# Optimization experiments

Hardware: AMD Instinct MI355X
Metric: run time of the kernel (lower is better)

Reference implementation:

```python
import jax, jax.numpy as jnp
import numpy as np

B, H = 4096, 1024
N1, N2, N3 = 28, 280, 2800  # nodes (== classes == paths) per level, branching [28,10,10]


def setup_inputs() -> dict:
    key = jax.random.key(0)
    ks = jax.random.split(key, 8)
    s = 1.0 / np.sqrt(H)  # torch nn.Linear default init bound
    x = jax.random.normal(ks[0], (B, H), jnp.float32)
    labels = jax.random.randint(ks[1], (B,), 0, N3, dtype=jnp.int32)
    W1 = jax.random.uniform(ks[2], (N1, H), jnp.float32, -s, s)
    b1 = jax.random.uniform(ks[3], (N1,), jnp.float32, -s, s)
    W2 = jax.random.uniform(ks[4], (N2, H), jnp.float32, -s, s)
    b2 = jax.random.uniform(ks[5], (N2,), jnp.float32, -s, s)
    W3 = jax.random.uniform(ks[6], (N3, H), jnp.float32, -s, s)
    b3 = jax.random.uniform(ks[7], (N3,), jnp.float32, -s, s)
    return {"x": x, "labels": labels, "W1": W1, "b1": b1,
            "W2": W2, "b2": b2, "W3": W3, "b3": b3}


def _ce(logits, lab):
    # mean cross-entropy, same as torch.nn.CrossEntropyLoss (mean reduction)
    lp = jax.nn.log_softmax(logits, axis=-1)
    return -jnp.take_along_axis(lp, lab[:, None], axis=1).mean()


def reference(x, labels, W1, b1, W2, b2, W3, b3):
    # per-level node probabilities: one grouped GEMM per level replaces the
    # Python loop of tiny Linear(hidden,1)+sigmoid calls
    z1 = jax.nn.sigmoid(x @ W1.T + b1)  # [B, N1]
    z2 = jax.nn.sigmoid(x @ W2.T + b2)  # [B, N2]
    z3 = jax.nn.sigmoid(x @ W3.T + b3)  # [B, N3]

    # path (prefix) matrices: leaf k has path [k//100, k//10, k].
    # NOTE: all nodes of a path index into the CURRENT level's weights,
    # exactly as self.nodes[lvl][node] does in the source.
    i2 = jnp.arange(N2)
    p2 = jnp.stack([i2 // 10, i2], axis=1)                    # [N2, 2]
    i3 = jnp.arange(N3)
    p3 = jnp.stack([i3 // 100, i3 // 10, i3], axis=1)          # [N3, 3]

    logits1 = z1                                               # prod over length-1 path
    logits2 = jnp.prod(z2[:, p2], axis=-1)                     # [B, N2]
    logits3 = jnp.prod(z3[:, p3], axis=-1)                     # [B, N3]

    # update_label_per_lvl: label -> ancestor node id at that level
    lab1 = labels // 100
    lab2 = labels // 10
    loss = _ce(logits1, lab1) + _ce(logits2, lab2) + _ce(logits3, labels)
    return logits3, loss
```

## Files before the change

kernel.cpp:

```cpp
#include <hip/hip_runtime.h>
#include <cstdint>


typedef unsigned short u16;
typedef unsigned char u8;
typedef long i64;
typedef float f32x4 __attribute__((ext_vector_type(4)));

#define AS_G __attribute__((address_space(1)))
#define AS_L __attribute__((address_space(3)))

constexpr int BATCH = 4096;
constexpr int H     = 1024;
constexpr int N1 = 28, N2 = 280, N3 = 2800;
constexpr int NT = N1 + N2 + N3;
constexpr int NP = 3200;
constexpr int NANC = N1 + N2 + 280;
constexpr float WSCALE = 16.0f;
constexpr float WINV   = 1.0f / 16.0f;

__device__ inline u16 f2bf(float f) {
    unsigned int u = __float_as_uint(f);
    u += 0x7fffu + ((u >> 16) & 1u);
    return (u16)(u >> 16);
}
__device__ inline float bf2f(unsigned int u) { return __uint_as_float(u << 16); }

__device__ inline unsigned int pk4_fp8(float a, float b, float c, float d) {
    unsigned int r = __builtin_amdgcn_cvt_pk_fp8_f32(a, b, 0, false);
    r = __builtin_amdgcn_cvt_pk_fp8_f32(c, d, (int)r, true);
    return r;
}

constexpr int XG = (BATCH * H) / 4;
constexpr int WG = (NP * H) / 4;
constexpr int BG = NP / 4;

__global__ __launch_bounds__(256) void cast_kernel(
        const float* __restrict__ x,
        const float* __restrict__ W1, const float* __restrict__ W2,
        const float* __restrict__ W3,
        const float* __restrict__ b1, const float* __restrict__ b2,
        const float* __restrict__ b3,
        u8* __restrict__ Xq, u8* __restrict__ Wq, float* __restrict__ biasf) {
    int g = blockIdx.x * 256 + threadIdx.x;
    if (g < XG) {
        float4 v = ((const float4*)x)[g];
        ((unsigned int*)Xq)[g] = pk4_fp8(v.x, v.y, v.z, v.w);
    } else if (g < XG + WG) {
        int wg = g - XG;
        int row = wg >> 8, cg = wg & 255;
        float4 v = make_float4(0.f, 0.f, 0.f, 0.f);
        if (row < N1)           v = ((const float4*)W1)[row * 256 + cg];
        else if (row < N1 + N2) v = ((const float4*)W2)[(row - N1) * 256 + cg];
        else if (row < NT)      v = ((const float4*)W3)[(row - N1 - N2) * 256 + cg];
        ((unsigned int*)Wq)[wg] = pk4_fp8(v.x * WSCALE, v.y * WSCALE, v.z * WSCALE, v.w * WSCALE);
    } else if (g < XG + WG + BG) {
        int bg = g - XG - WG;
        float4 v; float* vp = &v.x;
        #pragma unroll
        for (int i = 0; i < 4; ++i) {
            int c = bg * 4 + i; float t = 0.f;
            if (c < N1)           t = b1[c];
            else if (c < N1 + N2) t = b2[c - N1];
            else if (c < NT)      t = b3[c - N1 - N2];
            vp[i] = t;
        }
        ((float4*)biasf)[bg] = v;
    }
}

__global__ __launch_bounds__(256) void gemm_sig(
        const u8* __restrict__ Xq, const u8* __restrict__ Wq,
        const float* __restrict__ biasf, u16* __restrict__ Zb) {
    __shared__ __align__(16) u8 As[4 * 64 * 32];
    __shared__ __align__(16) u8 Bs[4 * 128 * 32];

    const int id  = blockIdx.x;
    const int xcd = id & 7;
    const int j   = id >> 3;
    const int m0 = ((xcd << 3) | (j & 7)) * 64;
    const int n0 = (j >> 3) * 128;

    const int tid  = threadIdx.x;
    const int lane = tid & 63;
    const int wave = tid >> 6;
    const int wr = wave >> 1;
    const int wc = wave & 1;

    const int laneM = lane & 15;
    const int u   = lane >> 4;
    const int xb  = (laneM >> 2) & 1;
    const int laneKb = (((u >> 1) ^ xb) << 4) + (u & 1) * 8;

    int arow[2], agoff[2];
    #pragma unroll
    for (int t = 0; t < 2; ++t) {
        const int c = tid + 256 * t;
        const int panel = c >> 7, rem = c & 127;
        const int row = rem >> 1, v = rem & 1;
        arow[t]  = row;
        agoff[t] = panel * 32 + ((v ^ ((row >> 2) & 1)) << 4);
    }
    int brow[4], bgoff[4];
    #pragma unroll
    for (int t = 0; t < 4; ++t) {
        const int c = tid + 256 * t;
        const int panel = c >> 8, rem = c & 255;
        const int row = rem >> 1, v = rem & 1;
        brow[t]  = row;
        bgoff[t] = panel * 32 + ((v ^ ((row >> 2) & 1)) << 4);
    }

    f32x4 acc[2][4] = {};

    for (int kt = 0; kt < H / 128; ++kt) {
        const int k0 = kt * 128;
        #pragma unroll
        for (int t = 0; t < 2; ++t) {
            const int c = tid + 256 * t;
            __builtin_amdgcn_global_load_lds(
                (const AS_G uint32_t*)(Xq + (size_t)(m0 + arow[t]) * H + k0 + agoff[t]),
                (AS_L uint32_t*)&As[c * 16], 16, 0, 0);
        }
        #pragma unroll
        for (int t = 0; t < 4; ++t) {
            const int c = tid + 256 * t;
            __builtin_amdgcn_global_load_lds(
                (const AS_G uint32_t*)(Wq + (size_t)(n0 + brow[t]) * H + k0 + bgoff[t]),
                (AS_L uint32_t*)&Bs[c * 16], 16, 0, 0);
        }
        __syncthreads();

        #pragma unroll
        for (int p = 0; p < 4; ++p) {
            i64 af[2], bfv[4];
            #pragma unroll
            for (int i = 0; i < 2; ++i)
                af[i]  = *(const i64*)&As[p * 2048 + (wr * 32 + i * 16 + laneM) * 32 + laneKb];
            #pragma unroll
            for (int i = 0; i < 4; ++i)
                bfv[i] = *(const i64*)&Bs[p * 4096 + (wc * 64 + i * 16 + laneM) * 32 + laneKb];
            #pragma unroll
            for (int am = 0; am < 2; ++am)
                #pragma unroll
                for (int bn = 0; bn < 4; ++bn)
                    acc[am][bn] = __builtin_amdgcn_mfma_f32_16x16x32_fp8_fp8(
                        af[am], bfv[bn], acc[am][bn], 0, 0, 0);
        }
        __syncthreads();
    }

    #pragma unroll
    for (int bn = 0; bn < 4; ++bn) {
        const int col = n0 + wc * 64 + bn * 16 + laneM;
        if (col >= NT) continue;
        const float bias = biasf[col];
        #pragma unroll
        for (int am = 0; am < 2; ++am) {
            const int rbase = m0 + wr * 32 + am * 16 + (lane >> 4) * 4;
            #pragma unroll
            for (int r = 0; r < 4; ++r) {
                float v = acc[am][bn][r] * WINV + bias;
                Zb[(size_t)(rbase + r) * NP + col] = f2bf(1.0f / (1.0f + __expf(-v)));
            }
        }
    }
}

__global__ __launch_bounds__(256) void logits_loss(
        const u16* __restrict__ Zb, const int* __restrict__ labels,
        float* __restrict__ out, float* __restrict__ partials) {
    __shared__ float zs[NANC];
    __shared__ float red[12];
    const int b = blockIdx.x, tid = threadIdx.x;
    const u16* Zrow = Zb + (size_t)b * NP;

    const unsigned int* Zr = (const unsigned int*)Zrow;
    for (int i = tid; i < NANC / 2; i += 256) {
        unsigned int v = Zr[i];
        zs[2 * i]     = bf2f(v & 0xffffu);
        zs[2 * i + 1] = bf2f(v >> 16);
    }
    __syncthreads();

    float se1 = 0.f, se2 = 0.f, se3 = 0.f;
    float4* outr4 = (float4*)(out + (size_t)b * N3);
    const uint2* Z3s = (const uint2*)(Zrow + N1 + N2);
    for (int q = tid; q < N3 / 4; q += 256) {
        const uint2 zv = Z3s[q];
        float z3v[4] = { bf2f(zv.x & 0xffffu), bf2f(zv.x >> 16),
                         bf2f(zv.y & 0xffffu), bf2f(zv.y >> 16) };
        const int k = q * 4;
        float4 o; float* op = &o.x;
        #pragma unroll
        for (int uu = 0; uu < 4; ++uu) {
            const int kk = k + uu;
            float lg = z3v[uu] * zs[308 + kk / 10] * zs[308 + kk / 100];
            op[uu] = lg;
            se3 += __expf(lg);
        }
        outr4[q] = o;
    }
    for (int jj = tid; jj < N2; jj += 256)
        se2 += __expf(zs[N1 + jj] * zs[N1 + jj / 10]);
    if (tid < N1)
        se1 = __expf(zs[tid]);

    #pragma unroll
    for (int off = 32; off > 0; off >>= 1) {
        se1 += __shfl_down(se1, off, 64);
        se2 += __shfl_down(se2, off, 64);
        se3 += __shfl_down(se3, off, 64);
    }
    if ((tid & 63) == 0) {
        int w = tid >> 6;
        red[w] = se3; red[4 + w] = se2; red[8 + w] = se1;
    }
    __syncthreads();
    if (tid == 0) {
        float s3 = red[0] + red[1] + red[2] + red[3];
        float s2 = red[4] + red[5] + red[6] + red[7];
        float s1 = red[8] + red[9] + red[10] + red[11];
        int lab  = labels[b];
        int lab2 = lab / 10, lab1 = lab / 100;
        float l1 = zs[lab1];
        float l2 = zs[N1 + lab2] * zs[N1 + lab2 / 10];
        float l3 = bf2f((unsigned int)Zrow[N1 + N2 + lab]) * zs[308 + lab2] * zs[308 + lab1];
        partials[b] = (logf(s1) - l1) + (logf(s2) - l2) + (logf(s3) - l3);
    }
}

__global__ __launch_bounds__(256) void final_reduce(
        const float* __restrict__ partials, float* __restrict__ out) {
    __shared__ float red[4];
    const int tid = threadIdx.x;
    float s = 0.f;
    for (int i = tid; i < BATCH; i += 256) s += partials[i];
    #pragma unroll
    for (int off = 32; off > 0; off >>= 1) s += __shfl_down(s, off, 64);
    if ((tid & 63) == 0) red[tid >> 6] = s;
    __syncthreads();
    if (tid == 0)
        out[(size_t)BATCH * N3] = (red[0] + red[1] + red[2] + red[3]) * (1.0f / BATCH);
}

extern "C" void kernel_launch(void* const* d_in, const int* in_sizes, int n_in,
                              void* d_out, int out_size, void* d_ws, size_t ws_size,
                              hipStream_t stream) {
    const float* x      = (const float*)d_in[0];
    const int*   labels = (const int*)d_in[1];
    const float* W1     = (const float*)d_in[2];
    const float* b1     = (const float*)d_in[3];
    const float* W2     = (const float*)d_in[4];
    const float* b2     = (const float*)d_in[5];
    const float* W3     = (const float*)d_in[6];
    const float* b3     = (const float*)d_in[7];
    float* out = (float*)d_out;

    char* ws = (char*)d_ws;
    u8*    Xq       = (u8*)ws;
    u8*    Wq       = (u8*)(ws + 4194304);
    u16*   Zb       = (u16*)(ws + 7471104);
    float* biasf    = (float*)(ws + 33685504);
    float* partials = (float*)(ws + 33698304);

    cast_kernel<<<(XG + WG + BG + 255) / 256, 256, 0, stream>>>(
        x, W1, W2, W3, b1, b2, b3, Xq, Wq, biasf);
    gemm_sig<<<1600, 256, 0, stream>>>(Xq, Wq, biasf, Zb);
    logits_loss<<<BATCH, 256, 0, stream>>>(Zb, labels, out, partials);
    final_reduce<<<1, 256, 0, stream>>>(partials, out);
}
```

Baseline: 144.5 us.

## Fuse level-3 sigmoid, path product and exp-sum into the level-3 GEMM epilogue

Splits the GEMM into a small ancestor GEMM (levels 1-2 plus the needed level-3 ancestor columns, 640 wide) and a level-3 GEMM. The level-3 GEMM epilogue computes the sigmoid, multiplies in ancestor probabilities staged in LDS, writes logits directly to the output and atomically accumulates per-row exp sums. This removes the full bf16 Z round trip through memory and the separate per-row logits pass. A lightweight CE kernel then does the level-1/2 terms and accumulates the loss atomically, which adds atomic traffic and makes the loss summation order nondeterministic.

```diff
diff --git a/kernel.cpp b/kernel.cpp
--- a/kernel.cpp
+++ b/kernel.cpp
@@ -15,9 +15,14 @@
 constexpr int N1 = 28, N2 = 280, N3 = 2800;
 constexpr int NT = N1 + N2 + N3;
 constexpr int NP = 3200;
-constexpr int NANC = N1 + N2 + 280;
+constexpr int NANCP = 640;
+constexpr int Z3OFF = N1 + N2;
 constexpr float WSCALE = 16.0f;
 constexpr float WINV   = 1.0f / 16.0f;
+
+constexpr int A10  = 14;
+constexpr int A100 = 3;
+constexpr int ANC100_BASE = 64 * A10;
 
 __device__ inline u16 f2bf(float f) {
     unsigned int u = __float_as_uint(f);
@@ -35,6 +40,8 @@
 constexpr int XG = (BATCH * H) / 4;
 constexpr int WG = (NP * H) / 4;
 constexpr int BG = NP / 4;
+constexpr int ZG = BATCH / 4;
+constexpr int TOTG = XG + WG + BG + ZG;
 
 __global__ __launch_bounds__(256) void cast_kernel(
         const float* __restrict__ x,
@@ -42,7 +49,8 @@
         const float* __restrict__ W3,
         const float* __restrict__ b1, const float* __restrict__ b2,
         const float* __restrict__ b3,
-        u8* __restrict__ Xq, u8* __restrict__ Wq, float* __restrict__ biasf) {
+        u8* __restrict__ Xq, u8* __restrict__ Wq, float* __restrict__ biasf,
+        float* __restrict__ sum3, float* __restrict__ loss_cell) {
     int g = blockIdx.x * 256 + threadIdx.x;
     if (g < XG) {
         float4 v = ((const float4*)x)[g];
@@ -67,12 +75,16 @@
             vp[i] = t;
         }
         ((float4*)biasf)[bg] = v;
-    }
-}
-
-__global__ __launch_bounds__(256) void gemm_sig(
+    } else if (g < TOTG) {
+        int zg = g - XG - WG - BG;
+        ((float4*)sum3)[zg] = make_float4(0.f, 0.f, 0.f, 0.f);
+        if (zg == 0) *loss_cell = 0.f;
+    }
+}
+
+__global__ __launch_bounds__(256) void gemm_anc(
         const u8* __restrict__ Xq, const u8* __restrict__ Wq,
-        const float* __restrict__ biasf, u16* __restrict__ Zb) {
+        const float* __restrict__ biasf, u16* __restrict__ Zanc) {
     __shared__ __align__(16) u8 As[4 * 64 * 32];
     __shared__ __align__(16) u8 Bs[4 * 128 * 32];
 
@@ -154,7 +166,6 @@
     #pragma unroll
     for (int bn = 0; bn < 4; ++bn) {
         const int col = n0 + wc * 64 + bn * 16 + laneM;
-        if (col >= NT) continue;
         const float bias = biasf[col];
         #pragma unroll
         for (int am = 0; am < 2; ++am) {
@@ -162,87 +173,175 @@
             #pragma unroll
             for (int r = 0; r < 4; ++r) {
                 float v = acc[am][bn][r] * WINV + bias;
-                Zb[(size_t)(rbase + r) * NP + col] = f2bf(1.0f / (1.0f + __expf(-v)));
+                Zanc[(size_t)(rbase + r) * NANCP + col] = f2bf(1.0f / (1.0f + __expf(-v)));
             }
         }
     }
 }
 
-__global__ __launch_bounds__(256) void logits_loss(
-        const u16* __restrict__ Zb, const int* __restrict__ labels,
-        float* __restrict__ out, float* __restrict__ partials) {
-    __shared__ float zs[NANC];
-    __shared__ float red[12];
-    const int b = blockIdx.x, tid = threadIdx.x;
-    const u16* Zrow = Zb + (size_t)b * NP;
-
-    const unsigned int* Zr = (const unsigned int*)Zrow;
-    for (int i = tid; i < NANC / 2; i += 256) {
-        unsigned int v = Zr[i];
-        zs[2 * i]     = bf2f(v & 0xffffu);
-        zs[2 * i + 1] = bf2f(v >> 16);
+__global__ __launch_bounds__(256) void gemm3(
+        const u8* __restrict__ Xq, const u8* __restrict__ Wq,
+        const float* __restrict__ biasf, const u16* __restrict__ Zanc,
+        float* __restrict__ out, float* __restrict__ sum3) {
+    __shared__ __align__(16) u8 As[4 * 64 * 32];
+    __shared__ __align__(16) u8 Bs[4 * 128 * 32];
+
+    const int id  = blockIdx.x;
+    const int xcd = id & 7;
+    const int j   = id >> 3;
+    const int m0 = ((xcd << 3) | (j & 7)) * 64;
+    const int c0 = (j >> 3) * 128;
+
+    const int tid  = threadIdx.x;
+    const int lane = tid & 63;
+    const int wave = tid >> 6;
+    const int wr = wave >> 1;
+    const int wc = wave & 1;
+
+    const int laneM = lane & 15;
+    const int u   = lane >> 4;
+    const int xb  = (laneM >> 2) & 1;
+    const int laneKb = (((u >> 1) ^ xb) << 4) + (u & 1) * 8;
+
+    int arow[2], agoff[2];
+    #pragma unroll
+    for (int t = 0; t < 2; ++t) {
+        const int c = tid + 256 * t;
+        const int panel = c >> 7, rem = c & 127;
+        const int row = rem >> 1, v = rem & 1;
+        arow[t]  = row;
+        agoff[t] = panel * 32 + ((v ^ ((row >> 2) & 1)) << 4);
+    }
+    int brow[4], bgoff[4];
+    #pragma unroll
+    for (int t = 0; t < 4; ++t) {
+        const int c = tid + 256 * t;
+        const int panel = c >> 8, rem = c & 255;
+        const int row = rem >> 1, v = rem & 1;
+        brow[t]  = row;
+        bgoff[t] = panel * 32 + ((v ^ ((row >> 2) & 1)) << 4);
+    }
+
+    f32x4 acc[2][4] = {};
+
+    for (int kt = 0; kt < H / 128; ++kt) {
+        const int k0 = kt * 128;
+        #pragma unroll
+        for (int t = 0; t < 2; ++t) {
+            const int c = tid + 256 * t;
+            __builtin_amdgcn_global_load_lds(
+                (const AS_G uint32_t*)(Xq + (size_t)(m0 + arow[t]) * H + k0 + agoff[t]),
+                (AS_L uint32_t*)&As[c * 16], 16, 0, 0);
+        }
+        #pragma unroll
+        for (int t = 0; t < 4; ++t) {
+            const int c = tid + 256 * t;
+            __builtin_amdgcn_global_load_lds(
+                (const AS_G uint32_t*)(Wq + (size_t)(Z3OFF + c0 + brow[t]) * H + k0 + bgoff[t]),
+                (AS_L uint32_t*)&Bs[c * 16], 16, 0, 0);
+        }
+        __syncthreads();
+
+        #pragma unroll
+        for (int p = 0; p < 4; ++p) {
+            i64 af[2], bfv[4];
+            #pragma unroll
+            for (int i = 0; i < 2; ++i)
+                af[i]  = *(const i64*)&As[p * 2048 + (wr * 32 + i * 16 + laneM) * 32 + laneKb];
+            #pragma unroll
+            for (int i = 0; i < 4; ++i)
+                bfv[i] = *(const i64*)&Bs[p * 4096 + (wc * 64 + i * 16 + laneM) * 32 + laneKb];
+            #pragma unroll
+            for (int am = 0; am < 2; ++am)
+                #pragma unroll
+                for (int bn = 0; bn < 4; ++bn)
+                    acc[am][bn] = __builtin_amdgcn_mfma_f32_16x16x32_fp8_fp8(
+                        af[am], bfv[bn], acc[am][bn], 0, 0, 0);
+        }
+        __syncthreads();
+    }
+
+    float* ancs = (float*)As;
+    const int j10  = c0 / 10;
+    const int j100 = c0 / 100;
+    for (int i = tid; i < 64 * A10; i += 256) {
+        int row = i / A10, jj = i - row * A10;
+        ancs[i] = bf2f((unsigned int)Zanc[(size_t)(m0 + row) * NANCP + Z3OFF + j10 + jj]);
+    }
+    if (tid < 64 * A100) {
+        int row = tid / A100, jj = tid - row * A100;
+        ancs[ANC100_BASE + tid] =
+            bf2f((unsigned int)Zanc[(size_t)(m0 + row) * NANCP + Z3OFF + j100 + jj]);
     }
     __syncthreads();
 
-    float se1 = 0.f, se2 = 0.f, se3 = 0.f;
-    float4* outr4 = (float4*)(out + (size_t)b * N3);
-    const uint2* Z3s = (const uint2*)(Zrow + N1 + N2);
-    for (int q = tid; q < N3 / 4; q += 256) {
-        const uint2 zv = Z3s[q];
-        float z3v[4] = { bf2f(zv.x & 0xffffu), bf2f(zv.x >> 16),
-                         bf2f(zv.y & 0xffffu), bf2f(zv.y >> 16) };
-        const int k = q * 4;
-        float4 o; float* op = &o.x;
-        #pragma unroll
-        for (int uu = 0; uu < 4; ++uu) {
-            const int kk = k + uu;
-            float lg = z3v[uu] * zs[308 + kk / 10] * zs[308 + kk / 100];
-            op[uu] = lg;
-            se3 += __expf(lg);
-        }
-        outr4[q] = o;
-    }
-    for (int jj = tid; jj < N2; jj += 256)
-        se2 += __expf(zs[N1 + jj] * zs[N1 + jj / 10]);
-    if (tid < N1)
-        se1 = __expf(zs[tid]);
-
+    float sume[2][4] = {};
+    #pragma unroll
+    for (int bn = 0; bn < 4; ++bn) {
+        const int colg = wc * 64 + bn * 16 + laneM;
+        const int k = c0 + colg;
+        const bool ok = k < N3;
+        const float bias = biasf[Z3OFF + k];
+        const int d10  = k / 10  - j10;
+        const int d100 = k / 100 - j100;
+        #pragma unroll
+        for (int am = 0; am < 2; ++am) {
+            const int rb = wr * 32 + am * 16 + u * 4;
+            #pragma unroll
+            for (int r = 0; r < 4; ++r) {
+                const int row = rb + r;
+                float v = acc[am][bn][r] * WINV + bias;
+                float z = 1.0f / (1.0f + __expf(-v));
+                float lg = z * ancs[row * A10 + d10] * ancs[ANC100_BASE + row * A100 + d100];
+                if (ok) {
+                    out[(size_t)(m0 + row) * N3 + k] = lg;
+                    sume[am][r] += __expf(lg);
+                }
+            }
+        }
+    }
+    #pragma unroll
+    for (int am = 0; am < 2; ++am)
+        #pragma unroll
+        for (int r = 0; r < 4; ++r) {
+            float s = sume[am][r];
+            s += __shfl_xor(s, 1, 64);
+            s += __shfl_xor(s, 2, 64);
+            s += __shfl_xor(s, 4, 64);
+            s += __shfl_xor(s, 8, 64);
+            if (laneM == 0)
+                atomicAdd(&sum3[m0 + wr * 32 + am * 16 + u * 4 + r], s);
+        }
+}
+
+__global__ __launch_bounds__(256) void ce_kernel(
+        const u16* __restrict__ Zanc, const float* __restrict__ out,
+        const int* __restrict__ labels, const float* __restrict__ sum3,
+        float* __restrict__ loss_cell) {
+    const int tid  = threadIdx.x;
+    const int lane = tid & 63;
+    const int b    = blockIdx.x * 4 + (tid >> 6);
+    const u16* Zr = Zanc + (size_t)b * NANCP;
+
+    float s1 = (lane < N1) ? __expf(bf2f((unsigned int)Zr[lane])) : 0.f;
+    float s2 = 0.f;
+    for (int jj = lane; jj < N2; jj += 64)
+        s2 += __expf(bf2f((unsigned int)Zr[N1 + jj]) * bf2f((unsigned int)Zr[N1 + jj / 10]));
     #pragma unroll
     for (int off = 32; off > 0; off >>= 1) {
-        se1 += __shfl_down(se1, off, 64);
-        se2 += __shfl_down(se2, off, 64);
-        se3 += __shfl_down(se3, off, 64);
-    }
-    if ((tid & 63) == 0) {
-        int w = tid >> 6;
-        red[w] = se3; red[4 + w] = se2; red[8 + w] = se1;
-    }
-    __syncthreads();
-    if (tid == 0) {
-        float s3 = red[0] + red[1] + red[2] + red[3];
-        float s2 = red[4] + red[5] + red[6] + red[7];
-        float s1 = red[8] + red[9] + red[10] + red[11];
-        int lab  = labels[b];
-        int lab2 = lab / 10, lab1 = lab / 100;
-        float l1 = zs[lab1];
-        float l2 = zs[N1 + lab2] * zs[N1 + lab2 / 10];
-        float l3 = bf2f((unsigned int)Zrow[N1 + N2 + lab]) * zs[308 + lab2] * zs[308 + lab1];
-        partials[b] = (logf(s1) - l1) + (logf(s2) - l2) + (logf(s3) - l3);
-    }
-}
-
-__global__ __launch_bounds__(256) void final_reduce(
-        const float* __restrict__ partials, float* __restrict__ out) {
-    __shared__ float red[4];
-    const int tid = threadIdx.x;
-    float s = 0.f;
-    for (int i = tid; i < BATCH; i += 256) s += partials[i];
-    #pragma unroll
-    for (int off = 32; off > 0; off >>= 1) s += __shfl_down(s, off, 64);
-    if ((tid & 63) == 0) red[tid >> 6] = s;
-    __syncthreads();
-    if (tid == 0)
-        out[(size_t)BATCH * N3] = (red[0] + red[1] + red[2] + red[3]) * (1.0f / BATCH);
+        s1 += __shfl_down(s1, off, 64);
+        s2 += __shfl_down(s2, off, 64);
+    }
+    if (lane == 0) {
+        const int lab  = labels[b];
+        const int lab2 = lab / 10, lab1 = lab / 100;
+        const float l1 = bf2f((unsigned int)Zr[lab1]);
+        const float l2 = bf2f((unsigned int)Zr[N1 + lab2]) * bf2f((unsigned int)Zr[N1 + lab2 / 10]);
+        const float l3 = out[(size_t)b * N3 + lab];
+        const float s3 = sum3[b];
+        const float partial = (logf(s1) - l1) + (logf(s2) - l2) + (logf(s3) - l3);
+        atomicAdd(loss_cell, partial * (1.0f / BATCH));
+    }
 }
 
 extern "C" void kernel_launch(void* const* d_in, const int* in_sizes, int n_in,
@@ -259,15 +358,16 @@
     float* out = (float*)d_out;
 
     char* ws = (char*)d_ws;
-    u8*    Xq       = (u8*)ws;
-    u8*    Wq       = (u8*)(ws + 4194304);
-    u16*   Zb       = (u16*)(ws + 7471104);
-    float* biasf    = (float*)(ws + 33685504);
-    float* partials = (float*)(ws + 33698304);
-
-    cast_kernel<<<(XG + WG + BG + 255) / 256, 256, 0, stream>>>(
-        x, W1, W2, W3, b1, b2, b3, Xq, Wq, biasf);
-    gemm_sig<<<1600, 256, 0, stream>>>(Xq, Wq, biasf, Zb);
-    logits_loss<<<BATCH, 256, 0, stream>>>(Zb, labels, out, partials);
-    final_reduce<<<1, 256, 0, stream>>>(partials, out);
-}
+    u8*    Xq    = (u8*)ws;
+    u8*    Wq    = (u8*)(ws + 4194304);
+    u16*   Zanc  = (u16*)(ws + 7471104);
+    float* biasf = (float*)(ws + 12713984);
+    float* sum3  = (float*)(ws + 12726784);
+    float* loss_cell = out + (size_t)BATCH * N3;
+
+    cast_kernel<<<(TOTG + 255) / 256, 256, 0, stream>>>(
+        x, W1, W2, W3, b1, b2, b3, Xq, Wq, biasf, sum3, loss_cell);
+    gemm_anc<<<320, 256, 0, stream>>>(Xq, Wq, biasf, Zanc);
+    gemm3<<<1408, 256, 0, stream>>>(Xq, Wq, biasf, Zanc, out, sum3);
+    ce_kernel<<<BATCH / 4, 256, 0, stream>>>(Zanc, out, labels, sum3, loss_cell);
+}
```

After: 206.8 us. +43.1%, slower.

## Double-buffer LDS tiles in fp8 GEMM with halved K step

Applied to the files above, without the earlier changes.

Splits the shared-memory A/B tiles into two buffers of half the K depth (64 instead of 128) and prefetches the next K slice into the alternate buffer while computing on the current one. The goal is to overlap global-to-LDS loads with the MFMA work, which the old load-sync-compute loop serialized. LDS footprint stays the same, but the loop now runs twice as many iterations, each still ending in a barrier. Overlap depends on the compiler not inserting a full vmcnt wait before the MFMA reads.

```diff
diff --git a/kernel.cpp b/kernel.cpp
--- a/kernel.cpp
+++ b/kernel.cpp
@@ -73,8 +73,8 @@
 __global__ __launch_bounds__(256) void gemm_sig(
         const u8* __restrict__ Xq, const u8* __restrict__ Wq,
         const float* __restrict__ biasf, u16* __restrict__ Zb) {
-    __shared__ __align__(16) u8 As[4 * 64 * 32];
-    __shared__ __align__(16) u8 Bs[4 * 128 * 32];
+    __shared__ __align__(16) u8 As[2][2 * 64 * 32];
+    __shared__ __align__(16) u8 Bs[2][2 * 128 * 32];
 
     const int id  = blockIdx.x;
     const int xcd = id & 7;
@@ -93,18 +93,13 @@
     const int xb  = (laneM >> 2) & 1;
     const int laneKb = (((u >> 1) ^ xb) << 4) + (u & 1) * 8;
 
-    int arow[2], agoff[2];
+    const int ac = tid;
+    const int apanel = ac >> 7, arem = ac & 127;
+    const int arowi = arem >> 1, av = arem & 1;
+    const int agoff = apanel * 32 + ((av ^ ((arowi >> 2) & 1)) << 4);
+    int brow[2], bgoff[2];
     #pragma unroll
     for (int t = 0; t < 2; ++t) {
-        const int c = tid + 256 * t;
-        const int panel = c >> 7, rem = c & 127;
-        const int row = rem >> 1, v = rem & 1;
-        arow[t]  = row;
-        agoff[t] = panel * 32 + ((v ^ ((row >> 2) & 1)) << 4);
-    }
-    int brow[4], bgoff[4];
-    #pragma unroll
-    for (int t = 0; t < 4; ++t) {
         const int c = tid + 256 * t;
         const int panel = c >> 8, rem = c & 255;
         const int row = rem >> 1, v = rem & 1;
@@ -112,35 +107,36 @@
         bgoff[t] = panel * 32 + ((v ^ ((row >> 2) & 1)) << 4);
     }
 
-    f32x4 acc[2][4] = {};
-
-    for (int kt = 0; kt < H / 128; ++kt) {
-        const int k0 = kt * 128;
+    auto STAGE = [&](int bufi, int kt) {
+        const int k0 = kt * 64;
+        __builtin_amdgcn_global_load_lds(
+            (const AS_G uint32_t*)(Xq + (size_t)(m0 + arowi) * H + k0 + agoff),
+            (AS_L uint32_t*)&As[bufi][ac * 16], 16, 0, 0);
         #pragma unroll
         for (int t = 0; t < 2; ++t) {
             const int c = tid + 256 * t;
             __builtin_amdgcn_global_load_lds(
-                (const AS_G uint32_t*)(Xq + (size_t)(m0 + arow[t]) * H + k0 + agoff[t]),
-                (AS_L uint32_t*)&As[c * 16], 16, 0, 0);
-        }
-        #pragma unroll
-        for (int t = 0; t < 4; ++t) {
-            const int c = tid + 256 * t;
-            __builtin_amdgcn_global_load_lds(
                 (const AS_G uint32_t*)(Wq + (size_t)(n0 + brow[t]) * H + k0 + bgoff[t]),
-                (AS_L uint32_t*)&Bs[c * 16], 16, 0, 0);
-        }
-        __syncthreads();
-
-        #pragma unroll
-        for (int p = 0; p < 4; ++p) {
+                (AS_L uint32_t*)&Bs[bufi][c * 16], 16, 0, 0);
+        }
+    };
+
+    f32x4 acc[2][4] = {};
+
+    STAGE(0, 0);
+    __syncthreads();
+    int buf = 0;
+    for (int kt = 0; kt < H / 64; ++kt) {
+        if (kt + 1 < H / 64) STAGE(buf ^ 1, kt + 1);
+        #pragma unroll
+        for (int p = 0; p < 2; ++p) {
             i64 af[2], bfv[4];
             #pragma unroll
             for (int i = 0; i < 2; ++i)
-                af[i]  = *(const i64*)&As[p * 2048 + (wr * 32 + i * 16 + laneM) * 32 + laneKb];
+                af[i]  = *(const i64*)&As[buf][p * 2048 + (wr * 32 + i * 16 + laneM) * 32 + laneKb];
             #pragma unroll
             for (int i = 0; i < 4; ++i)
-                bfv[i] = *(const i64*)&Bs[p * 4096 + (wc * 64 + i * 16 + laneM) * 32 + laneKb];
+                bfv[i] = *(const i64*)&Bs[buf][p * 4096 + (wc * 64 + i * 16 + laneM) * 32 + laneKb];
             #pragma unroll
             for (int am = 0; am < 2; ++am)
                 #pragma unroll
@@ -149,6 +145,7 @@
                         af[am], bfv[bn], acc[am][bn], 0, 0, 0);
         }
         __syncthreads();
+        buf ^= 1;
     }
 
     #pragma unroll
```

Result: slower. 149.4 us (+3.4%).
